# Optimization experiments

Hardware: AMD Instinct MI355X
Metric: run time of the kernel (lower is better)

## Reference

```python
import jax, jax.numpy as jnp
import numpy as np

V, E, H, W, S, T, B = 10000, 256, 512, 256, 512, 128, 64


def setup_inputs() -> dict:
    key = jax.random.key(0)
    ks = jax.random.split(key, 17)
    def rn(k, shape, s=0.08):
        return jax.random.normal(k, shape, jnp.float32) * s
    return {
        "tokens": jax.random.randint(ks[0], (B, S), 0, V),
        "dec_h0": jax.random.normal(ks[1], (B, H), jnp.float32),
        "emb_table": rn(ks[2], (V, E), 1.0),
        "enc_Wih": rn(ks[3], (4 * H, E)),
        "enc_Whh": rn(ks[4], (4 * H, H)),
        "enc_bih": rn(ks[5], (4 * H,)),
        "enc_bhh": rn(ks[6], (4 * H,)),
        "dec_Wih": rn(ks[7], (4 * H, E)),
        "dec_Whh": rn(ks[8], (4 * H, H)),
        "dec_bih": rn(ks[9], (4 * H,)),
        "dec_bhh": rn(ks[10], (4 * H,)),
        "W1_w": rn(ks[11], (W, H)),
        "W1_b": rn(ks[12], (W,)),
        "W2_w": rn(ks[13], (W, H)),
        "W2_b": rn(ks[14], (W,)),
        "vt_w": rn(ks[15], (1, W)),
        "vt_b": rn(ks[16], (1,)),
    }


def _lstm_cell(x, h, c, Wih, Whh, bih, bhh):
    # PyTorch gate order: input, forget, cell(g), output
    gates = x @ Wih.T + h @ Whh.T + bih + bhh
    i, f, g, o = jnp.split(gates, 4, axis=-1)
    c = jax.nn.sigmoid(f) * c + jax.nn.sigmoid(i) * jnp.tanh(g)
    h = jax.nn.sigmoid(o) * jnp.tanh(c)
    return h, c


def reference(tokens, dec_h0, emb_table, enc_Wih, enc_Whh, enc_bih, enc_bhh,
              dec_Wih, dec_Whh, dec_bih, dec_bhh, W1_w, W1_b, W2_w, W2_b,
              vt_w, vt_b):
    emb = emb_table[tokens]                       # [B,S,E]
    x_sbe = jnp.swapaxes(emb, 0, 1)               # [S,B,E] time-major
    bsz = tokens.shape[0]
    h0 = jnp.zeros((bsz, enc_Whh.shape[1]), emb.dtype)

    def enc_step(carry, x):
        h, c = carry
        h, c = _lstm_cell(x, h, c, enc_Wih, enc_Whh, enc_bih, enc_bhh)
        return (h, c), h

    _, enc_states = jax.lax.scan(enc_step, (h0, h0), x_sbe)   # [S,B,H]

    # W1(encoder_states) is constant across decoder steps -> hoist it
    blend1 = enc_states @ W1_w.T + W1_b            # [S,B,W]
    c0 = enc_states[-1]                            # original uses last enc state as cell init
    dec_in = jnp.zeros((bsz, emb_table.shape[1]), emb.dtype)  # never updated in original

    def dec_step(carry, _):
        h, c = carry
        h, c = _lstm_cell(dec_in, h, c, dec_Wih, dec_Whh, dec_bih, dec_bhh)
        blend2 = h @ W2_w.T + W2_b                 # [B,W]
        u = (jnp.tanh(blend1 + blend2[None]) @ vt_w.T)[..., 0] + vt_b[0]  # [S,B]
        logp = jax.nn.log_softmax(u.T, axis=1)     # [B,S], softmax over seq positions
        return (h, c), logp

    _, probs = jax.lax.scan(dec_step, (dec_h0, c0), None, length=T)  # [T,B,S]
    return jnp.swapaxes(probs, 0, 1)               # [B,T,S]
```

## Files before the change

kernel.cpp:

```cpp
#include <hip/hip_runtime.h>
#include <hip/hip_bf16.h>
#include <cstdint>
#include <cstddef>

typedef __bf16 bf16_t;
typedef __bf16 bf16x8 __attribute__((ext_vector_type(8)));
typedef float  f32x4  __attribute__((ext_vector_type(4)));

#define NB 64
#define NS 512
#define NTD 128
#define NE 256
#define NH 512
#define NG 2048
#define NW 256

#define HSTEP_DW 16384u

__device__ __forceinline__ float sigm_f(float x) { return 1.f / (1.f + __expf(-x)); }
__device__ __forceinline__ float tanh_f(float x) {
  float e = __expf(2.f * x);
  return 1.f - 2.f / (e + 1.f);
}
__device__ __forceinline__ float bits2f(uint32_t b16) {
  uint32_t u = b16 << 16;
  return __builtin_bit_cast(float, u);
}
__device__ __forceinline__ uint32_t packh(float a, float b) {
  uint16_t lo = __builtin_bit_cast(uint16_t, (bf16_t)a);
  uint16_t hi = __builtin_bit_cast(uint16_t, (bf16_t)b);
  return (uint32_t)lo | ((uint32_t)hi << 16);
}
__device__ __forceinline__ uint32_t aload(const uint32_t* p) {
  return __hip_atomic_load(p, __ATOMIC_RELAXED, __HIP_MEMORY_SCOPE_AGENT);
}
__device__ __forceinline__ uint64_t aload64(const uint64_t* p) {
  return __hip_atomic_load(p, __ATOMIC_RELAXED, __HIP_MEMORY_SCOPE_AGENT);
}
__device__ __forceinline__ void astore(uint32_t* p, uint32_t v) {
  __hip_atomic_store(p, v, __ATOMIC_RELAXED, __HIP_MEMORY_SCOPE_AGENT);
}

__global__ __launch_bounds__(256) void pack_all(
    const float* __restrict__ s0, bf16_t* __restrict__ d0,
    const float* __restrict__ s1, bf16_t* __restrict__ d1,
    const float* __restrict__ s2, bf16_t* __restrict__ d2,
    const float* __restrict__ s3, bf16_t* __restrict__ d3,
    const float* __restrict__ s4, bf16_t* __restrict__ d4) {
  int blk = blockIdx.x;
  const float* src; bf16_t* dst; int K, idx;
  if (blk < 2048)       { src = s0; dst = d0; K = 256; idx = blk * 256 + threadIdx.x; }
  else if (blk < 6144)  { src = s1; dst = d1; K = 512; idx = (blk - 2048) * 256 + threadIdx.x; }
  else if (blk < 10240) { src = s2; dst = d2; K = 512; idx = (blk - 6144) * 256 + threadIdx.x; }
  else if (blk < 10752) { src = s3; dst = d3; K = 512; idx = (blk - 10240) * 256 + threadIdx.x; }
  else                  { src = s4; dst = d4; K = 512; idx = (blk - 10752) * 256 + threadIdx.x; }
  int n = idx / K, k = idx - n * K;
  int lane = (((k & 31) >> 3) << 4) | (n & 15);
  size_t o = ((((size_t)(n >> 4) * (K >> 5)) + (k >> 5)) * 64 + lane) * 8 + (k & 7);
  dst[o] = (bf16_t)src[idx];
}

__global__ __launch_bounds__(256) void gather_emb2(
    const int* __restrict__ tokens, const float* __restrict__ table,
    bf16_t* __restrict__ embfrag, const float* __restrict__ dec_h0,
    uint32_t* __restrict__ dec_hf0) {
  int blk = blockIdx.x;
  if (blk < 4096) {
    int idx = blk * 256 + threadIdx.x;
    int row = idx >> 5, e0 = (idx & 31) << 3;
    int b = row & 63, s = row >> 6;
    int tok = tokens[b * NS + s];
    const float4* p = (const float4*)(table + (size_t)tok * NE + e0);
    float4 v0 = p[0], v1 = p[1];
    bf16x8 v;
    v[0] = (bf16_t)v0.x; v[1] = (bf16_t)v0.y; v[2] = (bf16_t)v0.z; v[3] = (bf16_t)v0.w;
    v[4] = (bf16_t)v1.x; v[5] = (bf16_t)v1.y; v[6] = (bf16_t)v1.z; v[7] = (bf16_t)v1.w;
    int mt = row >> 4;
    int ks = e0 >> 5;
    int lane = (b & 15) | (((e0 >> 3) & 3) << 4);
    *(bf16x8*)(embfrag + ((size_t)(mt * 8 + ks) * 64 + lane) * 8) = v;
  } else {
    int idx = (blk - 4096) * 256 + threadIdx.x;
    int b = idx >> 8, jp = idx & 255;
    int j = jp * 2;
    float lo = dec_h0[(size_t)b * NH + j], hi = dec_h0[(size_t)b * NH + j + 1];
    int bg = b >> 4, bl = b & 15, ks = j >> 5;
    int lane = bl | (((j >> 3) & 3) << 4);
    dec_hf0[((size_t)bg * 16 + ks) * 256 + lane * 4 + ((j >> 1) & 3)] = packh(lo, hi);
  }
}

template <typename OutT, int KS, int MT>
__global__ __launch_bounds__(256) void gemm_fa2(const bf16_t* __restrict__ A,
                                                const bf16_t* __restrict__ Bp,
                                                OutT* __restrict__ out,
                                                const float* __restrict__ bias1,
                                                const float* __restrict__ bias2,
                                                int N) {
  int lane = threadIdx.x & 63, w = threadIdx.x >> 6;
  int nt = blockIdx.x * 4 + w;
  int mt0 = blockIdx.y * MT;
  bf16x8 bfr[KS];
  const bf16_t* bp = Bp + ((size_t)nt * KS * 64 + lane) * 8;
#pragma unroll
  for (int ks = 0; ks < KS; ++ks) bfr[ks] = *(const bf16x8*)(bp + (size_t)ks * 512);
  int col = (nt << 4) + (lane & 15);
  float bs = bias1[col] + (bias2 ? bias2[col] : 0.f);
  for (int m = 0; m < MT; ++m) {
    int mt = mt0 + m;
    const bf16_t* ap = A + (size_t)mt * (KS * 512) + lane * 8;
    f32x4 acc = {0.f, 0.f, 0.f, 0.f};
#pragma unroll
    for (int ks = 0; ks < KS; ++ks)
      acc = __builtin_amdgcn_mfma_f32_16x16x32_bf16(
          *(const bf16x8*)(ap + (size_t)ks * 512), bfr[ks], acc, 0, 0, 0);
    int rbase = (mt << 4) + ((lane >> 4) << 2);
#pragma unroll
    for (int r = 0; r < 4; ++r)
      out[(size_t)(rbase + r) * N + col] = (OutT)(acc[r] + bs);
  }
}

__global__ __launch_bounds__(256) void lstm_chain_enc(
    const bf16_t* __restrict__ Wp, const bf16_t* __restrict__ xih,
    uint32_t* __restrict__ hfrag, uint32_t* __restrict__ flags) {
  __shared__ bf16_t wlds[8 * 8192];
  __shared__ float gl[4][16][36];
  int tid = threadIdx.x, lane = tid & 63, wv = tid >> 6;
  int bg = blockIdx.x >> 4, slice = blockIdx.x & 15;

  for (int l = 0; l < 8; ++l) {
    int g = l >> 1, p = l & 1;
    const bf16_t* src = Wp + (size_t)(g * 32 + slice * 2 + p) * 8192;
    bf16_t* dst = wlds + (size_t)l * 8192;
    for (int i = tid; i < 1024; i += 256)
      *(bf16x8*)(dst + (size_t)i * 8) = *(const bf16x8*)(src + (size_t)i * 8);
  }

  int ub = tid >> 4, uj2 = tid & 15;
  int lane_f = ub | ((uj2 >> 2) << 4);
  float c0 = 0.f, c1 = 0.f;
  __syncthreads();

  const uint64_t* hq = (const uint64_t*)hfrag;
  uint32_t* fl = flags + bg * 16;

  for (int t = 0; t < NS; ++t) {
    uint32_t xd[4];
    {
      const uint32_t* xr = (const uint32_t*)xih +
          ((size_t)(t * 64 + bg * 16 + ub)) * 1024 + slice * 16 + uj2;
#pragma unroll
      for (int g = 0; g < 4; ++g) xd[g] = xr[(size_t)g * 256];
    }
    if (t > 0) {
      uint32_t tgt = (uint32_t)t;
      bool ok;
      do {
        uint32_t f = tgt;
        if (lane < 16 && lane != (uint32_t)slice) f = aload(fl + lane);
        ok = __all(f >= tgt);
      } while (!ok);
    }
    const uint64_t* hb = hq + ((size_t)t * 4 + bg) * 2048 + lane * 2;
    uint64_t aq[16][2];
#pragma unroll
    for (int ks = 0; ks < 16; ++ks) {
      aq[ks][0] = aload64(hb + (size_t)ks * 128);
      aq[ks][1] = aload64(hb + (size_t)ks * 128 + 1);
    }
    const bf16_t* wl = wlds + (size_t)(wv * 2) * 8192 + lane * 8;
    f32x4 acc0 = {0.f, 0.f, 0.f, 0.f}, acc1 = {0.f, 0.f, 0.f, 0.f};
#pragma unroll
    for (int ks = 0; ks < 16; ++ks) {
      union { uint64_t q[2]; bf16x8 v; } u;
      u.q[0] = aq[ks][0]; u.q[1] = aq[ks][1];
      acc0 = __builtin_amdgcn_mfma_f32_16x16x32_bf16(
          u.v, *(const bf16x8*)(wl + (size_t)ks * 512), acc0, 0, 0, 0);
      acc1 = __builtin_amdgcn_mfma_f32_16x16x32_bf16(
          u.v, *(const bf16x8*)(wl + 8192 + (size_t)ks * 512), acc1, 0, 0, 0);
    }
    int cc = lane & 15, rb = (lane >> 4) << 2;
#pragma unroll
    for (int r = 0; r < 4; ++r) {
      gl[wv][rb + r][cc] = acc0[r];
      gl[wv][rb + r][16 + cc] = acc1[r];
    }
    __syncthreads();

    float p[4][2];
#pragma unroll
    for (int g = 0; g < 4; ++g) {
      p[g][0] = gl[g][ub][uj2 * 2] + bits2f(xd[g] & 0xffffu);
      p[g][1] = gl[g][ub][uj2 * 2 + 1] + bits2f(xd[g] >> 16);
    }
    float i0 = sigm_f(p[0][0]), f0 = sigm_f(p[1][0]);
    float g0 = tanh_f(p[2][0]), o0 = sigm_f(p[3][0]);
    c0 = f0 * c0 + i0 * g0;
    float h0 = o0 * tanh_f(c0);
    float i1 = sigm_f(p[0][1]), f1 = sigm_f(p[1][1]);
    float g1 = tanh_f(p[2][1]), o1 = sigm_f(p[3][1]);
    c1 = f1 * c1 + i1 * g1;
    float h1 = o1 * tanh_f(c1);
    astore(hfrag + ((size_t)(t + 1) * 4 + bg) * 4096 +
               slice * 256 + lane_f * 4 + (uj2 & 3), packh(h0, h1));
    __syncthreads();
    if (tid == 0) astore(fl + slice, (uint32_t)(t + 1));
  }
}

__global__ __launch_bounds__(256) void lstm_chain_dec(
    const bf16_t* __restrict__ Wp, const float* __restrict__ bih,
    const float* __restrict__ bhh, uint32_t* __restrict__ hfrag,
    const uint32_t* __restrict__ c0frag, uint32_t* __restrict__ flags) {
  __shared__ bf16_t wlds[8 * 8192];
  __shared__ float gl[4][16][36];
  int tid = threadIdx.x, lane = tid & 63, wv = tid >> 6;
  int bg = blockIdx.x >> 4, slice = blockIdx.x & 15;

  for (int l = 0; l < 8; ++l) {
    int g = l >> 1, p = l & 1;
    const bf16_t* src = Wp + (size_t)(g * 32 + slice * 2 + p) * 8192;
    bf16_t* dst = wlds + (size_t)l * 8192;
    for (int i = tid; i < 1024; i += 256)
      *(bf16x8*)(dst + (size_t)i * 8) = *(const bf16x8*)(src + (size_t)i * 8);
  }
  int ub = tid >> 4, uj2 = tid & 15;
  int j_lo = slice * 32 + uj2 * 2;
  int lane_f = ub | ((uj2 >> 2) << 4);
  uint32_t d = c0frag[((size_t)bg * 16 + slice) * 256 + lane_f * 4 + (uj2 & 3)];
  float c0 = bits2f(d & 0xffffu), c1 = bits2f(d >> 16);
  float bsum[4][2];
#pragma unroll
  for (int g = 0; g < 4; ++g) {
    bsum[g][0] = bih[g * NH + j_lo] + bhh[g * NH + j_lo];
    bsum[g][1] = bih[g * NH + j_lo + 1] + bhh[g * NH + j_lo + 1];
  }
  __syncthreads();

  const uint64_t* hq = (const uint64_t*)hfrag;
  uint32_t* fl = flags + bg * 16;

  for (int t = 0; t < NTD; ++t) {
    if (t > 0) {
      uint32_t tgt = (uint32_t)t;
      bool ok;
      do {
        uint32_t f = tgt;
        if (lane < 16 && lane != (uint32_t)slice) f = aload(fl + lane);
        ok = __all(f >= tgt);
      } while (!ok);
    }
    const uint64_t* hb = hq + ((size_t)t * 4 + bg) * 2048 + lane * 2;
    uint64_t aq[16][2];
#pragma unroll
    for (int ks = 0; ks < 16; ++ks) {
      aq[ks][0] = aload64(hb + (size_t)ks * 128);
      aq[ks][1] = aload64(hb + (size_t)ks * 128 + 1);
    }
    const bf16_t* wl = wlds + (size_t)(wv * 2) * 8192 + lane * 8;
    f32x4 acc0 = {0.f, 0.f, 0.f, 0.f}, acc1 = {0.f, 0.f, 0.f, 0.f};
#pragma unroll
    for (int ks = 0; ks < 16; ++ks) {
      union { uint64_t q[2]; bf16x8 v; } u;
      u.q[0] = aq[ks][0]; u.q[1] = aq[ks][1];
      acc0 = __builtin_amdgcn_mfma_f32_16x16x32_bf16(
          u.v, *(const bf16x8*)(wl + (size_t)ks * 512), acc0, 0, 0, 0);
      acc1 = __builtin_amdgcn_mfma_f32_16x16x32_bf16(
          u.v, *(const bf16x8*)(wl + 8192 + (size_t)ks * 512), acc1, 0, 0, 0);
    }
    int cc = lane & 15, rb = (lane >> 4) << 2;
#pragma unroll
    for (int r = 0; r < 4; ++r) {
      gl[wv][rb + r][cc] = acc0[r];
      gl[wv][rb + r][16 + cc] = acc1[r];
    }
    __syncthreads();

    float p[4][2];
#pragma unroll
    for (int g = 0; g < 4; ++g) {
      p[g][0] = gl[g][ub][uj2 * 2] + bsum[g][0];
      p[g][1] = gl[g][ub][uj2 * 2 + 1] + bsum[g][1];
    }
    float i0 = sigm_f(p[0][0]), f0 = sigm_f(p[1][0]);
    float g0 = tanh_f(p[2][0]), o0 = sigm_f(p[3][0]);
    c0 = f0 * c0 + i0 * g0;
    float h0 = o0 * tanh_f(c0);
    float i1 = sigm_f(p[0][1]), f1 = sigm_f(p[1][1]);
    float g1 = tanh_f(p[2][1]), o1 = sigm_f(p[3][1]);
    c1 = f1 * c1 + i1 * g1;
    float h1 = o1 * tanh_f(c1);
    astore(hfrag + ((size_t)(t + 1) * 4 + bg) * 4096 +
               slice * 256 + lane_f * 4 + (uj2 & 3), packh(h0, h1));
    __syncthreads();
    if (tid == 0) astore(fl + slice, (uint32_t)(t + 1));
  }
}

__global__ __launch_bounds__(256) void attn_v2(const bf16_t* __restrict__ blend1,
                                               const float* __restrict__ blend2,
                                               const float* __restrict__ vt_w,
                                               float* __restrict__ out) {
  __shared__ float s_u[512], s_red[8];
  int t = blockIdx.x >> 6, b = blockIdx.x & 63;
  int tid = threadIdx.x, lane = tid & 63, wv = tid >> 6;
  int sslot = lane >> 4, wseg = lane & 15;
  int w0 = wseg * 16;

  float vt[16], b2[16];
  {
    const float4* vp = (const float4*)(vt_w + w0);
    const float4* bp = (const float4*)(blend2 + (size_t)(t * 64 + b) * NW + w0);
#pragma unroll
    for (int i = 0; i < 4; ++i) {
      float4 a = vp[i], c = bp[i];
      vt[i * 4 + 0] = a.x; vt[i * 4 + 1] = a.y; vt[i * 4 + 2] = a.z; vt[i * 4 + 3] = a.w;
      b2[i * 4 + 0] = c.x; b2[i * 4 + 1] = c.y; b2[i * 4 + 2] = c.z; b2[i * 4 + 3] = c.w;
    }
  }
  for (int p = 0; p < 32; ++p) {
    int s = p * 16 + wv * 4 + sslot;
    const bf16_t* row = blend1 + ((size_t)s * NB + b) * NW + w0;
    bf16x8 v0 = *(const bf16x8*)(row);
    bf16x8 v1 = *(const bf16x8*)(row + 8);
    float val = 0.f;
#pragma unroll
    for (int k = 0; k < 8; ++k) val += vt[k] * tanh_f((float)v0[k] + b2[k]);
#pragma unroll
    for (int k = 0; k < 8; ++k) val += vt[8 + k] * tanh_f((float)v1[k] + b2[8 + k]);
    val += __shfl_xor(val, 1, 64);
    val += __shfl_xor(val, 2, 64);
    val += __shfl_xor(val, 4, 64);
    val += __shfl_xor(val, 8, 64);
    if (wseg == 0) s_u[s] = val;
  }
  __syncthreads();
  float a = s_u[tid], bb2 = s_u[tid + 256];
  float m = fmaxf(a, bb2);
#pragma unroll
  for (int o = 1; o < 64; o <<= 1) m = fmaxf(m, __shfl_xor(m, o, 64));
  if (lane == 0) s_red[wv] = m;
  __syncthreads();
  m = fmaxf(fmaxf(s_red[0], s_red[1]), fmaxf(s_red[2], s_red[3]));
  float e = __expf(a - m) + __expf(bb2 - m);
#pragma unroll
  for (int o = 1; o < 64; o <<= 1) e += __shfl_xor(e, o, 64);
  if (lane == 0) s_red[4 + wv] = e;
  __syncthreads();
  float lz = m + logf(s_red[4] + s_red[5] + s_red[6] + s_red[7]);
  size_t ob = ((size_t)b * NTD + t) * NS;
  out[ob + tid] = a - lz;
  out[ob + tid + 256] = bb2 - lz;
}

extern "C" void kernel_launch(void* const* d_in, const int* in_sizes, int n_in,
                              void* d_out, int out_size, void* d_ws, size_t ws_size,
                              hipStream_t stream) {
  const int*   tokens    = (const int*)d_in[0];
  const float* dec_h0    = (const float*)d_in[1];
  const float* emb_table = (const float*)d_in[2];
  const float* enc_Wih   = (const float*)d_in[3];
  const float* enc_Whh   = (const float*)d_in[4];
  const float* enc_bih   = (const float*)d_in[5];
  const float* enc_bhh   = (const float*)d_in[6];
  const float* dec_Whh   = (const float*)d_in[8];
  const float* dec_bih   = (const float*)d_in[9];
  const float* dec_bhh   = (const float*)d_in[10];
  const float* W1_w      = (const float*)d_in[11];
  const float* W1_b      = (const float*)d_in[12];
  const float* W2_w      = (const float*)d_in[13];
  const float* W2_b      = (const float*)d_in[14];
  const float* vt_w      = (const float*)d_in[15];
  float* out = (float*)d_out;

  char* w = (char*)d_ws;
  size_t off = 0;
  auto alloc = [&](size_t bytes) {
    size_t o = off;
    off += (bytes + 255) & ~(size_t)255;
    return o;
  };
  bf16_t* embfrag = (bf16_t*)(w + alloc((size_t)NS * NB * NE * 2));
  bf16_t* xih     = (bf16_t*)(w + alloc((size_t)NS * NB * NG * 2));
  uint32_t* enc_hf = (uint32_t*)(w + alloc((size_t)(NS + 1) * HSTEP_DW * 4));
  uint32_t* dec_hf = (uint32_t*)(w + alloc((size_t)(NTD + 1) * HSTEP_DW * 4));
  bf16_t* blend1  = (bf16_t*)(w + alloc((size_t)NS * NB * NW * 2));
  float*  blend2  = (float*)(w + alloc((size_t)NTD * NB * NW * 4));
  bf16_t* pWih    = (bf16_t*)(w + alloc((size_t)NG * NE * 2));
  bf16_t* pWhhE   = (bf16_t*)(w + alloc((size_t)NG * NH * 2));
  bf16_t* pWhhD   = (bf16_t*)(w + alloc((size_t)NG * NH * 2));
  bf16_t* pW1     = (bf16_t*)(w + alloc((size_t)NW * NH * 2));
  bf16_t* pW2     = (bf16_t*)(w + alloc((size_t)NW * NH * 2));
  uint32_t* flags = (uint32_t*)(w + alloc(512));
  (void)ws_size; (void)in_sizes; (void)n_in; (void)out_size;

  hipMemsetAsync(flags, 0, 512, stream);
  hipMemsetAsync(enc_hf, 0, HSTEP_DW * 4, stream);

  pack_all<<<11264, 256, 0, stream>>>(enc_Wih, pWih, enc_Whh, pWhhE,
                                      dec_Whh, pWhhD, W1_w, pW1, W2_w, pW2);

  gather_emb2<<<4160, 256, 0, stream>>>(tokens, emb_table, embfrag, dec_h0, dec_hf);

  gemm_fa2<bf16_t, 8, 16><<<dim3(128 / 4, 2048 / 16), 256, 0, stream>>>(
      embfrag, pWih, xih, enc_bih, enc_bhh, NG);

  lstm_chain_enc<<<64, 256, 0, stream>>>(pWhhE, xih, enc_hf, flags);

  gemm_fa2<bf16_t, 16, 16><<<dim3(16 / 4, 2048 / 16), 256, 0, stream>>>(
      (const bf16_t*)(enc_hf + HSTEP_DW), pW1, blend1, W1_b, nullptr, NW);

  lstm_chain_dec<<<64, 256, 0, stream>>>(pWhhD, dec_bih, dec_bhh, dec_hf,
                                         enc_hf + (size_t)NS * HSTEP_DW,
                                         flags + 64);

  gemm_fa2<float, 16, 16><<<dim3(16 / 4, 512 / 16), 256, 0, stream>>>(
      (const bf16_t*)(dec_hf + HSTEP_DW), pW2, blend2, W2_b, nullptr, NW);

  attn_v2<<<NTD * NB, 256, 0, stream>>>(blend1, blend2, vt_w, out);
}
```

Measured before the change: 2.804 ms.

## Compute all four LSTM gates per wave in registers, drop LDS gate exchange

The recurrent LSTM kernels now use 128 threads, and each wave computes all four gate tiles for its 16 hidden units. The cell update therefore runs directly on the MFMA accumulators, with no LDS round trip and one fewer block barrier per step. A new xih GEMM writes input projections in a fragment-matched layout, so each lane loads its gate inputs as contiguous uint2 values. The trade-off is fewer waves per block, with more serial MFMAs per wave on the latency-critical recurrence.

```diff
diff --git a/kernel.cpp b/kernel.cpp
--- a/kernel.cpp
+++ b/kernel.cpp
@@ -39,6 +39,10 @@
 }
 __device__ __forceinline__ void astore(uint32_t* p, uint32_t v) {
   __hip_atomic_store(p, v, __ATOMIC_RELAXED, __HIP_MEMORY_SCOPE_AGENT);
+}
+__device__ __forceinline__ float xpick(uint2 v, int r) {
+  uint32_t d = (r < 2) ? v.x : v.y;
+  return bits2f((r & 1) ? (d >> 16) : (d & 0xffffu));
 }
 
 __global__ __launch_bounds__(256) void pack_all(
@@ -121,38 +125,72 @@
   }
 }
 
-__global__ __launch_bounds__(256) void lstm_chain_enc(
-    const bf16_t* __restrict__ Wp, const bf16_t* __restrict__ xih,
+__global__ __launch_bounds__(256) void gemm_xih(const bf16_t* __restrict__ A,
+                                                const bf16_t* __restrict__ Bp,
+                                                bf16_t* __restrict__ out,
+                                                const float* __restrict__ b1,
+                                                const float* __restrict__ b2) {
+  const int KS = 8, MT = 16;
+  int lane = threadIdx.x & 63, w = threadIdx.x >> 6;
+  int nt = blockIdx.x * 4 + w;
+  int mt0 = blockIdx.y * MT;
+  bf16x8 bfr[KS];
+  const bf16_t* bp = Bp + ((size_t)nt * KS * 64 + lane) * 8;
+#pragma unroll
+  for (int ks = 0; ks < KS; ++ks) bfr[ks] = *(const bf16x8*)(bp + (size_t)ks * 512);
+  int n = (nt << 4) + (lane & 15);
+  float bs = b1[n] + b2[n];
+  int g = nt >> 5, sl = (nt & 31) >> 1, ct = nt & 1;
+  for (int m = 0; m < MT; ++m) {
+    int mt = mt0 + m;
+    const bf16_t* ap = A + (size_t)mt * (KS * 512) + lane * 8;
+    f32x4 acc = {0.f, 0.f, 0.f, 0.f};
+#pragma unroll
+    for (int ks = 0; ks < KS; ++ks)
+      acc = __builtin_amdgcn_mfma_f32_16x16x32_bf16(
+          *(const bf16x8*)(ap + (size_t)ks * 512), bfr[ks], acc, 0, 0, 0);
+    ushort4 hv;
+    hv.x = __builtin_bit_cast(uint16_t, (bf16_t)(acc[0] + bs));
+    hv.y = __builtin_bit_cast(uint16_t, (bf16_t)(acc[1] + bs));
+    hv.z = __builtin_bit_cast(uint16_t, (bf16_t)(acc[2] + bs));
+    hv.w = __builtin_bit_cast(uint16_t, (bf16_t)(acc[3] + bs));
+    *(ushort4*)(out + ((((size_t)mt * 16 + sl) * 2 + ct) * 4 + g) * 256 + lane * 4) = hv;
+  }
+}
+
+__global__ __launch_bounds__(128) void lstm_chain_enc(
+    const bf16_t* __restrict__ Wp, const bf16_t* __restrict__ xih2,
     uint32_t* __restrict__ hfrag, uint32_t* __restrict__ flags) {
   __shared__ bf16_t wlds[8 * 8192];
-  __shared__ float gl[4][16][36];
-  int tid = threadIdx.x, lane = tid & 63, wv = tid >> 6;
+  int tid = threadIdx.x, lane = tid & 63, ct = tid >> 6;
   int bg = blockIdx.x >> 4, slice = blockIdx.x & 15;
 
   for (int l = 0; l < 8; ++l) {
     int g = l >> 1, p = l & 1;
-    const bf16_t* src = Wp + (size_t)(g * 32 + slice * 2 + p) * 8192;
-    bf16_t* dst = wlds + (size_t)l * 8192;
-    for (int i = tid; i < 1024; i += 256)
-      *(bf16x8*)(dst + (size_t)i * 8) = *(const bf16x8*)(src + (size_t)i * 8);
-  }
-
-  int ub = tid >> 4, uj2 = tid & 15;
-  int lane_f = ub | ((uj2 >> 2) << 4);
-  float c0 = 0.f, c1 = 0.f;
+    const bf16_t* s = Wp + (size_t)(g * 32 + slice * 2 + p) * 8192;
+    for (int i = tid; i < 1024; i += 128)
+      *(bf16x8*)(wlds + l * 8192 + (size_t)i * 8) = *(const bf16x8*)(s + (size_t)i * 8);
+  }
   __syncthreads();
 
   const uint64_t* hq = (const uint64_t*)hfrag;
   uint32_t* fl = flags + bg * 16;
+  int c = lane & 15, grp = lane >> 4;
+  int j = slice * 32 + ct * 16 + c;
+  int sub = (j >> 3) & 3, dw = (j >> 1) & 3;
+  float cst[4] = {0.f, 0.f, 0.f, 0.f};
+  const bf16_t* wb0 = wlds + (size_t)(0 * 2 + ct) * 8192;
+  const bf16_t* wb1 = wlds + (size_t)(1 * 2 + ct) * 8192;
+  const bf16_t* wb2 = wlds + (size_t)(2 * 2 + ct) * 8192;
+  const bf16_t* wb3 = wlds + (size_t)(3 * 2 + ct) * 8192;
 
   for (int t = 0; t < NS; ++t) {
-    uint32_t xd[4];
-    {
-      const uint32_t* xr = (const uint32_t*)xih +
-          ((size_t)(t * 64 + bg * 16 + ub)) * 1024 + slice * 16 + uj2;
-#pragma unroll
-      for (int g = 0; g < 4; ++g) xd[g] = xr[(size_t)g * 256];
-    }
+    const uint32_t* xb = (const uint32_t*)xih2 +
+        ((((size_t)t * 4 + bg) * 16 + slice) * 2 + ct) * 512 + lane * 2;
+    uint2 xg0 = *(const uint2*)(xb);
+    uint2 xg1 = *(const uint2*)(xb + 128);
+    uint2 xg2 = *(const uint2*)(xb + 256);
+    uint2 xg3 = *(const uint2*)(xb + 384);
     if (t > 0) {
       uint32_t tgt = (uint32_t)t;
       bool ok;
@@ -169,77 +207,73 @@
       aq[ks][0] = aload64(hb + (size_t)ks * 128);
       aq[ks][1] = aload64(hb + (size_t)ks * 128 + 1);
     }
-    const bf16_t* wl = wlds + (size_t)(wv * 2) * 8192 + lane * 8;
-    f32x4 acc0 = {0.f, 0.f, 0.f, 0.f}, acc1 = {0.f, 0.f, 0.f, 0.f};
+    f32x4 a0 = {0.f,0.f,0.f,0.f}, a1 = a0, a2 = a0, a3 = a0;
 #pragma unroll
     for (int ks = 0; ks < 16; ++ks) {
       union { uint64_t q[2]; bf16x8 v; } u;
       u.q[0] = aq[ks][0]; u.q[1] = aq[ks][1];
-      acc0 = __builtin_amdgcn_mfma_f32_16x16x32_bf16(
-          u.v, *(const bf16x8*)(wl + (size_t)ks * 512), acc0, 0, 0, 0);
-      acc1 = __builtin_amdgcn_mfma_f32_16x16x32_bf16(
-          u.v, *(const bf16x8*)(wl + 8192 + (size_t)ks * 512), acc1, 0, 0, 0);
-    }
-    int cc = lane & 15, rb = (lane >> 4) << 2;
+      int o = ks * 512 + lane * 8;
+      a0 = __builtin_amdgcn_mfma_f32_16x16x32_bf16(u.v, *(const bf16x8*)(wb0 + o), a0, 0, 0, 0);
+      a1 = __builtin_amdgcn_mfma_f32_16x16x32_bf16(u.v, *(const bf16x8*)(wb1 + o), a1, 0, 0, 0);
+      a2 = __builtin_amdgcn_mfma_f32_16x16x32_bf16(u.v, *(const bf16x8*)(wb2 + o), a2, 0, 0, 0);
+      a3 = __builtin_amdgcn_mfma_f32_16x16x32_bf16(u.v, *(const bf16x8*)(wb3 + o), a3, 0, 0, 0);
+    }
+    uint32_t hsb = ((uint32_t)(t + 1) * 4 + (uint32_t)bg) * 4096 + slice * 256;
 #pragma unroll
     for (int r = 0; r < 4; ++r) {
-      gl[wv][rb + r][cc] = acc0[r];
-      gl[wv][rb + r][16 + cc] = acc1[r];
-    }
-    __syncthreads();
-
-    float p[4][2];
-#pragma unroll
-    for (int g = 0; g < 4; ++g) {
-      p[g][0] = gl[g][ub][uj2 * 2] + bits2f(xd[g] & 0xffffu);
-      p[g][1] = gl[g][ub][uj2 * 2 + 1] + bits2f(xd[g] >> 16);
-    }
-    float i0 = sigm_f(p[0][0]), f0 = sigm_f(p[1][0]);
-    float g0 = tanh_f(p[2][0]), o0 = sigm_f(p[3][0]);
-    c0 = f0 * c0 + i0 * g0;
-    float h0 = o0 * tanh_f(c0);
-    float i1 = sigm_f(p[0][1]), f1 = sigm_f(p[1][1]);
-    float g1 = tanh_f(p[2][1]), o1 = sigm_f(p[3][1]);
-    c1 = f1 * c1 + i1 * g1;
-    float h1 = o1 * tanh_f(c1);
-    astore(hfrag + ((size_t)(t + 1) * 4 + bg) * 4096 +
-               slice * 256 + lane_f * 4 + (uj2 & 3), packh(h0, h1));
+      float pi = a0[r] + xpick(xg0, r), pf = a1[r] + xpick(xg1, r);
+      float pg = a2[r] + xpick(xg2, r), po = a3[r] + xpick(xg3, r);
+      float iG = sigm_f(pi), fG = sigm_f(pf), gG = tanh_f(pg), oG = sigm_f(po);
+      cst[r] = fG * cst[r] + iG * gG;
+      float h = oG * tanh_f(cst[r]);
+      uint16_t hv = __builtin_bit_cast(uint16_t, (bf16_t)h);
+      uint32_t other = (uint32_t)__shfl_xor((int)(uint32_t)hv, 1, 64);
+      if (!(lane & 1)) {
+        uint32_t dword = (uint32_t)hv | (other << 16);
+        astore(hfrag + (size_t)hsb + (((grp * 4 + r) | (sub << 4)) * 4 + dw), dword);
+      }
+    }
     __syncthreads();
     if (tid == 0) astore(fl + slice, (uint32_t)(t + 1));
   }
 }
 
-__global__ __launch_bounds__(256) void lstm_chain_dec(
+__global__ __launch_bounds__(128) void lstm_chain_dec(
     const bf16_t* __restrict__ Wp, const float* __restrict__ bih,
     const float* __restrict__ bhh, uint32_t* __restrict__ hfrag,
     const uint32_t* __restrict__ c0frag, uint32_t* __restrict__ flags) {
   __shared__ bf16_t wlds[8 * 8192];
-  __shared__ float gl[4][16][36];
-  int tid = threadIdx.x, lane = tid & 63, wv = tid >> 6;
+  int tid = threadIdx.x, lane = tid & 63, ct = tid >> 6;
   int bg = blockIdx.x >> 4, slice = blockIdx.x & 15;
 
   for (int l = 0; l < 8; ++l) {
     int g = l >> 1, p = l & 1;
-    const bf16_t* src = Wp + (size_t)(g * 32 + slice * 2 + p) * 8192;
-    bf16_t* dst = wlds + (size_t)l * 8192;
-    for (int i = tid; i < 1024; i += 256)
-      *(bf16x8*)(dst + (size_t)i * 8) = *(const bf16x8*)(src + (size_t)i * 8);
-  }
-  int ub = tid >> 4, uj2 = tid & 15;
-  int j_lo = slice * 32 + uj2 * 2;
-  int lane_f = ub | ((uj2 >> 2) << 4);
-  uint32_t d = c0frag[((size_t)bg * 16 + slice) * 256 + lane_f * 4 + (uj2 & 3)];
-  float c0 = bits2f(d & 0xffffu), c1 = bits2f(d >> 16);
-  float bsum[4][2];
-#pragma unroll
-  for (int g = 0; g < 4; ++g) {
-    bsum[g][0] = bih[g * NH + j_lo] + bhh[g * NH + j_lo];
-    bsum[g][1] = bih[g * NH + j_lo + 1] + bhh[g * NH + j_lo + 1];
+    const bf16_t* s = Wp + (size_t)(g * 32 + slice * 2 + p) * 8192;
+    for (int i = tid; i < 1024; i += 128)
+      *(bf16x8*)(wlds + l * 8192 + (size_t)i * 8) = *(const bf16x8*)(s + (size_t)i * 8);
   }
   __syncthreads();
 
   const uint64_t* hq = (const uint64_t*)hfrag;
   uint32_t* fl = flags + bg * 16;
+  int c = lane & 15, grp = lane >> 4;
+  int j = slice * 32 + ct * 16 + c;
+  int sub = (j >> 3) & 3, dw = (j >> 1) & 3, half = j & 1;
+  float bs0 = bih[0 * NH + j] + bhh[0 * NH + j];
+  float bs1 = bih[1 * NH + j] + bhh[1 * NH + j];
+  float bs2 = bih[2 * NH + j] + bhh[2 * NH + j];
+  float bs3 = bih[3 * NH + j] + bhh[3 * NH + j];
+  float cst[4];
+#pragma unroll
+  for (int r = 0; r < 4; ++r) {
+    uint32_t d = c0frag[(size_t)(bg * 16 + slice) * 256 +
+                        (((grp * 4 + r) | (sub << 4)) * 4 + dw)];
+    cst[r] = half ? bits2f(d >> 16) : bits2f(d & 0xffffu);
+  }
+  const bf16_t* wb0 = wlds + (size_t)(0 * 2 + ct) * 8192;
+  const bf16_t* wb1 = wlds + (size_t)(1 * 2 + ct) * 8192;
+  const bf16_t* wb2 = wlds + (size_t)(2 * 2 + ct) * 8192;
+  const bf16_t* wb3 = wlds + (size_t)(3 * 2 + ct) * 8192;
 
   for (int t = 0; t < NTD; ++t) {
     if (t > 0) {
@@ -258,41 +292,31 @@
       aq[ks][0] = aload64(hb + (size_t)ks * 128);
       aq[ks][1] = aload64(hb + (size_t)ks * 128 + 1);
     }
-    const bf16_t* wl = wlds + (size_t)(wv * 2) * 8192 + lane * 8;
-    f32x4 acc0 = {0.f, 0.f, 0.f, 0.f}, acc1 = {0.f, 0.f, 0.f, 0.f};
+    f32x4 a0 = {0.f,0.f,0.f,0.f}, a1 = a0, a2 = a0, a3 = a0;
 #pragma unroll
     for (int ks = 0; ks < 16; ++ks) {
       union { uint64_t q[2]; bf16x8 v; } u;
       u.q[0] = aq[ks][0]; u.q[1] = aq[ks][1];
-      acc0 = __builtin_amdgcn_mfma_f32_16x16x32_bf16(
-          u.v, *(const bf16x8*)(wl + (size_t)ks * 512), acc0, 0, 0, 0);
-      acc1 = __builtin_amdgcn_mfma_f32_16x16x32_bf16(
-          u.v, *(const bf16x8*)(wl + 8192 + (size_t)ks * 512), acc1, 0, 0, 0);
-    }
-    int cc = lane & 15, rb = (lane >> 4) << 2;
+      int o = ks * 512 + lane * 8;
+      a0 = __builtin_amdgcn_mfma_f32_16x16x32_bf16(u.v, *(const bf16x8*)(wb0 + o), a0, 0, 0, 0);
+      a1 = __builtin_amdgcn_mfma_f32_16x16x32_bf16(u.v, *(const bf16x8*)(wb1 + o), a1, 0, 0, 0);
+      a2 = __builtin_amdgcn_mfma_f32_16x16x32_bf16(u.v, *(const bf16x8*)(wb2 + o), a2, 0, 0, 0);
+      a3 = __builtin_amdgcn_mfma_f32_16x16x32_bf16(u.v, *(const bf16x8*)(wb3 + o), a3, 0, 0, 0);
+    }
+    uint32_t hsb = ((uint32_t)(t + 1) * 4 + (uint32_t)bg) * 4096 + slice * 256;
 #pragma unroll
     for (int r = 0; r < 4; ++r) {
-      gl[wv][rb + r][cc] = acc0[r];
-      gl[wv][rb + r][16 + cc] = acc1[r];
-    }
-    __syncthreads();
-
-    float p[4][2];
-#pragma unroll
-    for (int g = 0; g < 4; ++g) {
-      p[g][0] = gl[g][ub][uj2 * 2] + bsum[g][0];
-      p[g][1] = gl[g][ub][uj2 * 2 + 1] + bsum[g][1];
-    }
-    float i0 = sigm_f(p[0][0]), f0 = sigm_f(p[1][0]);
-    float g0 = tanh_f(p[2][0]), o0 = sigm_f(p[3][0]);
-    c0 = f0 * c0 + i0 * g0;
-    float h0 = o0 * tanh_f(c0);
-    float i1 = sigm_f(p[0][1]), f1 = sigm_f(p[1][1]);
-    float g1 = tanh_f(p[2][1]), o1 = sigm_f(p[3][1]);
-    c1 = f1 * c1 + i1 * g1;
-    float h1 = o1 * tanh_f(c1);
-    astore(hfrag + ((size_t)(t + 1) * 4 + bg) * 4096 +
-               slice * 256 + lane_f * 4 + (uj2 & 3), packh(h0, h1));
+      float iG = sigm_f(a0[r] + bs0), fG = sigm_f(a1[r] + bs1);
+      float gG = tanh_f(a2[r] + bs2), oG = sigm_f(a3[r] + bs3);
+      cst[r] = fG * cst[r] + iG * gG;
+      float h = oG * tanh_f(cst[r]);
+      uint16_t hv = __builtin_bit_cast(uint16_t, (bf16_t)h);
+      uint32_t other = (uint32_t)__shfl_xor((int)(uint32_t)hv, 1, 64);
+      if (!(lane & 1)) {
+        uint32_t dword = (uint32_t)hv | (other << 16);
+        astore(hfrag + (size_t)hsb + (((grp * 4 + r) | (sub << 4)) * 4 + dw), dword);
+      }
+    }
     __syncthreads();
     if (tid == 0) astore(fl + slice, (uint32_t)(t + 1));
   }
@@ -382,7 +406,7 @@
     return o;
   };
   bf16_t* embfrag = (bf16_t*)(w + alloc((size_t)NS * NB * NE * 2));
-  bf16_t* xih     = (bf16_t*)(w + alloc((size_t)NS * NB * NG * 2));
+  bf16_t* xih2    = (bf16_t*)(w + alloc((size_t)NS * NB * NG * 2));
   uint32_t* enc_hf = (uint32_t*)(w + alloc((size_t)(NS + 1) * HSTEP_DW * 4));
   uint32_t* dec_hf = (uint32_t*)(w + alloc((size_t)(NTD + 1) * HSTEP_DW * 4));
   bf16_t* blend1  = (bf16_t*)(w + alloc((size_t)NS * NB * NW * 2));
@@ -403,15 +427,15 @@
 
   gather_emb2<<<4160, 256, 0, stream>>>(tokens, emb_table, embfrag, dec_h0, dec_hf);
 
-  gemm_fa2<bf16_t, 8, 16><<<dim3(128 / 4, 2048 / 16), 256, 0, stream>>>(
-      embfrag, pWih, xih, enc_bih, enc_bhh, NG);
-
-  lstm_chain_enc<<<64, 256, 0, stream>>>(pWhhE, xih, enc_hf, flags);
+  gemm_xih<<<dim3(128 / 4, 2048 / 16), 256, 0, stream>>>(
+      embfrag, pWih, xih2, enc_bih, enc_bhh);
+
+  lstm_chain_enc<<<64, 128, 0, stream>>>(pWhhE, xih2, enc_hf, flags);
 
   gemm_fa2<bf16_t, 16, 16><<<dim3(16 / 4, 2048 / 16), 256, 0, stream>>>(
       (const bf16_t*)(enc_hf + HSTEP_DW), pW1, blend1, W1_b, nullptr, NW);
 
-  lstm_chain_dec<<<64, 256, 0, stream>>>(pWhhD, dec_bih, dec_bhh, dec_hf,
+  lstm_chain_dec<<<64, 128, 0, stream>>>(pWhhD, dec_bih, dec_bhh, dec_hf,
                                          enc_hf + (size_t)NS * HSTEP_DW,
                                          flags + 64);
 
```

Measured after the change: 3.135 ms. 11.8% more time.

## Stage GEMM outputs through LDS for coalesced stores and merge blend GEMMs

Applied to the files above, without the earlier changes.

The xih GEMM and the two blend GEMMs now write their MFMA results into a shared-memory tile first, then emit coalesced 8- or 16-byte row stores instead of scattered per-element stores. The W1 and W2 projection GEMMs are merged into one launch placed after the decoder chain, which removes a launch and lets both run in a single grid. The cost is two extra block barriers per M-tile. Moving the W1 GEMM after the decoder also removes any chance of it overlapping with the decoder chain.

```diff
diff --git a/kernel.cpp b/kernel.cpp
--- a/kernel.cpp
+++ b/kernel.cpp
@@ -90,13 +90,13 @@
   }
 }
 
-template <typename OutT, int KS, int MT>
-__global__ __launch_bounds__(256) void gemm_fa2(const bf16_t* __restrict__ A,
-                                                const bf16_t* __restrict__ Bp,
-                                                OutT* __restrict__ out,
-                                                const float* __restrict__ bias1,
-                                                const float* __restrict__ bias2,
-                                                int N) {
+__global__ __launch_bounds__(256) void gemm_xih_st(const bf16_t* __restrict__ A,
+                                                   const bf16_t* __restrict__ Bp,
+                                                   bf16_t* __restrict__ out,
+                                                   const float* __restrict__ b1,
+                                                   const float* __restrict__ b2) {
+  __shared__ bf16_t tile[16][68];
+  const int KS = 8, MT = 16;
   int lane = threadIdx.x & 63, w = threadIdx.x >> 6;
   int nt = blockIdx.x * 4 + w;
   int mt0 = blockIdx.y * MT;
@@ -105,7 +105,9 @@
 #pragma unroll
   for (int ks = 0; ks < KS; ++ks) bfr[ks] = *(const bf16x8*)(bp + (size_t)ks * 512);
   int col = (nt << 4) + (lane & 15);
-  float bs = bias1[col] + (bias2 ? bias2[col] : 0.f);
+  float bs = b1[col] + b2[col];
+  int row0 = (lane >> 4) << 2;
+  int rw = threadIdx.x >> 4, ch = threadIdx.x & 15;
   for (int m = 0; m < MT; ++m) {
     int mt = mt0 + m;
     const bf16_t* ap = A + (size_t)mt * (KS * 512) + lane * 8;
@@ -114,10 +116,64 @@
     for (int ks = 0; ks < KS; ++ks)
       acc = __builtin_amdgcn_mfma_f32_16x16x32_bf16(
           *(const bf16x8*)(ap + (size_t)ks * 512), bfr[ks], acc, 0, 0, 0);
-    int rbase = (mt << 4) + ((lane >> 4) << 2);
 #pragma unroll
     for (int r = 0; r < 4; ++r)
-      out[(size_t)(rbase + r) * N + col] = (OutT)(acc[r] + bs);
+      tile[row0 + r][w * 16 + (lane & 15)] = (bf16_t)(acc[r] + bs);
+    __syncthreads();
+    ushort4 v = *(const ushort4*)&tile[rw][ch * 4];
+    *(ushort4*)(out + (size_t)(mt * 16 + rw) * NG + blockIdx.x * 64 + ch * 4) = v;
+    __syncthreads();
+  }
+}
+
+__global__ __launch_bounds__(256) void gemm_blends(
+    const bf16_t* __restrict__ encA, const bf16_t* __restrict__ W1p,
+    const float* __restrict__ W1_b, bf16_t* __restrict__ blend1,
+    const bf16_t* __restrict__ decA, const bf16_t* __restrict__ W2p,
+    const float* __restrict__ W2_b, float* __restrict__ blend2) {
+  union { bf16_t t16[16][68]; float t32[16][68]; } sm;
+  __shared__ decltype(sm) tile;
+  const int KS = 16;
+  int lane = threadIdx.x & 63, w = threadIdx.x >> 6;
+  int nt = blockIdx.x * 4 + w;
+  bool is1 = blockIdx.y < 128;
+  int mt0 = (is1 ? blockIdx.y : (blockIdx.y - 128)) * 16;
+  const bf16_t* A  = is1 ? encA : decA;
+  const bf16_t* Bp = is1 ? W1p : W2p;
+  const float* bias = is1 ? W1_b : W2_b;
+  bf16x8 bfr[KS];
+  const bf16_t* bp = Bp + ((size_t)nt * KS * 64 + lane) * 8;
+#pragma unroll
+  for (int ks = 0; ks < KS; ++ks) bfr[ks] = *(const bf16x8*)(bp + (size_t)ks * 512);
+  int col = (nt << 4) + (lane & 15);
+  float bs = bias[col];
+  int row0 = (lane >> 4) << 2;
+  int rw = threadIdx.x >> 4, ch = threadIdx.x & 15;
+  for (int m = 0; m < 16; ++m) {
+    int mt = mt0 + m;
+    const bf16_t* ap = A + (size_t)mt * (KS * 512) + lane * 8;
+    f32x4 acc = {0.f, 0.f, 0.f, 0.f};
+#pragma unroll
+    for (int ks = 0; ks < KS; ++ks)
+      acc = __builtin_amdgcn_mfma_f32_16x16x32_bf16(
+          *(const bf16x8*)(ap + (size_t)ks * 512), bfr[ks], acc, 0, 0, 0);
+    if (is1) {
+#pragma unroll
+      for (int r = 0; r < 4; ++r)
+        tile.t16[row0 + r][w * 16 + (lane & 15)] = (bf16_t)(acc[r] + bs);
+      __syncthreads();
+      ushort4 v = *(const ushort4*)&tile.t16[rw][ch * 4];
+      *(ushort4*)(blend1 + (size_t)(mt * 16 + rw) * NW + blockIdx.x * 64 + ch * 4) = v;
+      __syncthreads();
+    } else {
+#pragma unroll
+      for (int r = 0; r < 4; ++r)
+        tile.t32[row0 + r][w * 16 + (lane & 15)] = acc[r] + bs;
+      __syncthreads();
+      float4 v = *(const float4*)&tile.t32[rw][ch * 4];
+      *(float4*)(blend2 + (size_t)(mt * 16 + rw) * NW + blockIdx.x * 64 + ch * 4) = v;
+      __syncthreads();
+    }
   }
 }
 
@@ -403,20 +459,18 @@
 
   gather_emb2<<<4160, 256, 0, stream>>>(tokens, emb_table, embfrag, dec_h0, dec_hf);
 
-  gemm_fa2<bf16_t, 8, 16><<<dim3(128 / 4, 2048 / 16), 256, 0, stream>>>(
-      embfrag, pWih, xih, enc_bih, enc_bhh, NG);
+  gemm_xih_st<<<dim3(32, 128), 256, 0, stream>>>(embfrag, pWih, xih,
+                                                 enc_bih, enc_bhh);
 
   lstm_chain_enc<<<64, 256, 0, stream>>>(pWhhE, xih, enc_hf, flags);
-
-  gemm_fa2<bf16_t, 16, 16><<<dim3(16 / 4, 2048 / 16), 256, 0, stream>>>(
-      (const bf16_t*)(enc_hf + HSTEP_DW), pW1, blend1, W1_b, nullptr, NW);
 
   lstm_chain_dec<<<64, 256, 0, stream>>>(pWhhD, dec_bih, dec_bhh, dec_hf,
                                          enc_hf + (size_t)NS * HSTEP_DW,
                                          flags + 64);
 
-  gemm_fa2<float, 16, 16><<<dim3(16 / 4, 512 / 16), 256, 0, stream>>>(
-      (const bf16_t*)(dec_hf + HSTEP_DW), pW2, blend2, W2_b, nullptr, NW);
+  gemm_blends<<<dim3(4, 160), 256, 0, stream>>>(
+      (const bf16_t*)(enc_hf + HSTEP_DW), pW1, W1_b, blend1,
+      (const bf16_t*)(dec_hf + HSTEP_DW), pW2, W2_b, blend2);
 
   attn_v2<<<NTD * NB, 256, 0, stream>>>(blend1, blend2, vt_w, out);
 }
```

New measurement: 2.826 ms. About the same (+0.8%).
